# Kernel optimization log

Measured on AMD Instinct MI355X. Metric: run time of the kernel, lower is better.

## Reference

```python
import jax, jax.numpy as jnp
import numpy as np

B, L, D = 8, 2048, 512


def setup_inputs() -> dict:
    key = jax.random.key(0)
    ks = jax.random.split(key, 9)
    s = 1.0 / np.sqrt(D)
    x = jax.random.normal(ks[0], (B, L, D), dtype=jnp.float32)
    Wq = jax.random.uniform(ks[1], (D, D), jnp.float32, -s, s)
    bq = jax.random.uniform(ks[2], (D,), jnp.float32, -s, s)
    Wk = jax.random.uniform(ks[3], (D, D), jnp.float32, -s, s)
    bk = jax.random.uniform(ks[4], (D,), jnp.float32, -s, s)
    Wv = jax.random.uniform(ks[5], (D, D), jnp.float32, -s, s)
    bv = jax.random.uniform(ks[6], (D,), jnp.float32, -s, s)
    Wo = jax.random.uniform(ks[7], (D, D), jnp.float32, -s, s)
    bo = jax.random.uniform(ks[8], (D,), jnp.float32, -s, s)
    return {"x": x, "Wq": Wq, "bq": bq, "Wk": Wk, "bk": bk,
            "Wv": Wv, "bv": bv, "Wo": Wo, "bo": bo}


def reference(x, Wq, bq, Wk, bk, Wv, bv, Wo, bo):
    # Projections then rfft along sequence axis -> complex [B, F, D], F = L//2+1
    Q = jnp.fft.rfft(x @ Wq + bq, axis=1)
    K = jnp.fft.rfft(x @ Wk + bk, axis=1)
    V = jnp.fft.rfft(x @ Wv + bv, axis=1)
    scale = K.shape[-1] ** (-0.5)
    # Complex attention scores over frequency bins: [B, F, F]
    att = jnp.einsum('bfd,bgd->bfg', Q, K) * scale
    attn = jax.nn.softmax(jnp.abs(att), axis=-1)
    context = jnp.einsum('bfg,bgd->bfd', attn.astype(Q.dtype), V)
    context = jnp.fft.irfft(context, n=x.shape[1], axis=1)  # [B, L, D] real
    return context @ Wo + bo
```

## Files before the change

kernel.cpp:

```cpp
#include <hip/hip_runtime.h>
#include <hip/hip_bf16.h>
#include <math.h>

typedef __hip_bfloat16 bf16;
typedef __attribute__((ext_vector_type(8))) short short8;
typedef __attribute__((ext_vector_type(4))) float f32x4;

#define BB 8
#define LL 2048
#define DD 512
#define FF 1025
#define GP 1088
#define FPAD 1152
#define PSTRIDE 589824
#define ATT_SCALE 0.04419417382415922f

__device__ __forceinline__ float b2f(bf16 v) { return __bfloat162float(v); }
__device__ __forceinline__ bf16  f2b(float v) { return __float2bfloat16(v); }
__device__ __forceinline__ float s2f(short s) { bf16 t; *reinterpret_cast<short*>(&t) = s; return b2f(t); }
__device__ __forceinline__ unsigned pk2f(float a, float b) {
    bf16 ha = f2b(a), hb = f2b(b);
    return (unsigned)*(unsigned short*)&ha | ((unsigned)*(unsigned short*)&hb << 16);
}

#define MFMA16(a, b, c) __builtin_amdgcn_mfma_f32_16x16x32_bf16((a), (b), (c), 0, 0, 0)

__device__ __forceinline__ short8 neg8(short8 v) {
    short8 r;
    #pragma unroll
    for (int t = 0; t < 8; ++t) r[t] = (short)(v[t] ^ (short)0x8000);
    return r;
}

typedef __attribute__((address_space(1))) const unsigned int gu32;
typedef __attribute__((address_space(3))) unsigned int lu32;
__device__ __forceinline__ void gl16(const void* g, void* l) {
    __builtin_amdgcn_global_load_lds((gu32*)g, (lu32*)l, 16, 0, 0);
}

template<bool F32>
__device__ __forceinline__ float ldin(const void* p, size_t i) {
    if (F32) return ((const float*)p)[i];
    else     return b2f(((const bf16*)p)[i]);
}

__global__ __launch_bounds__(256) void detect_dtype(const unsigned short* __restrict__ x,
                                                    int* __restrict__ flag)
{
    __shared__ int cnt[256];
    int c = 0;
    for (int i = threadIdx.x; i < 4096; i += 256) {
        const int e = (x[i] >> 7) & 0xFF;
        c += (e >= 100 && e <= 150) ? 1 : 0;
    }
    cnt[threadIdx.x] = c;
    __syncthreads();
    for (int s = 128; s; s >>= 1) {
        if (threadIdx.x < s) cnt[threadIdx.x] += cnt[threadIdx.x + s];
        __syncthreads();
    }
    if (threadIdx.x == 0) *flag = (cnt[0] < 3400) ? 1 : 0;
}

__global__ __launch_bounds__(256) void prep_bias(const void* __restrict__ b0,
                                                 const void* __restrict__ b1,
                                                 const void* __restrict__ b2,
                                                 const void* __restrict__ b3,
                                                 float* __restrict__ bias_f,
                                                 const int* __restrict__ flag)
{
    const int idx = blockIdx.x * 256 + threadIdx.x;
    const int which = idx >> 9, i = idx & 511;
    const void* src = which == 0 ? b0 : (which == 1 ? b1 : (which == 2 ? b2 : b3));
    bias_f[idx] = (*flag) ? ldin<true>(src, i) : ldin<false>(src, i);
}

__global__ __launch_bounds__(256) void split_w_t(const void* __restrict__ W0,
                                                 const void* __restrict__ W1,
                                                 const void* __restrict__ W2,
                                                 const void* __restrict__ W3,
                                                 bf16* __restrict__ WT,
                                                 const int* __restrict__ flag)
{
    const int z = blockIdx.z;
    const void* W = z == 0 ? W0 : (z == 1 ? W1 : (z == 2 ? W2 : W3));
    bf16* Wh = WT + (size_t)z * 524288;
    const int k0 = blockIdx.x * 32, n0 = blockIdx.y * 32;
    const bool f32 = (*flag) != 0;
    __shared__ float Tl[32][33];
    for (int it = 0; it < 4; ++it) {
        const int idx = it * 256 + threadIdx.x;
        const int lk = idx >> 5, ln = idx & 31;
        Tl[lk][ln] = f32 ? ldin<true>(W, (size_t)(k0 + lk) * 512 + n0 + ln)
                         : ldin<false>(W, (size_t)(k0 + lk) * 512 + n0 + ln);
    }
    __syncthreads();
    for (int it = 0; it < 4; ++it) {
        const int idx = it * 256 + threadIdx.x;
        const int ln = idx >> 5, lk = idx & 31;
        Wh[(size_t)(n0 + ln) * 512 + k0 + lk] = f2b(Tl[lk][ln]);
    }
}

__device__ __forceinline__ int shx(int i, int c) {
    const int x = (i << 2) | c;
    return x ^ (((x >> 6) & 3) << 2);
}

__device__ __forceinline__ void fft_decode(int flat, int& b, int& dp) {
    const int c8 = flat & 7;
    const int s  = (flat >> 3) & 1;
    const int pp = flat >> 4;
    const int idx = c8 * 32 + pp;
    b  = idx >> 5;
    dp = ((idx & 31) << 1) | s;
}

__device__ __forceinline__ void fill_twl(float2* twl, int tid) {
    for (int idx = tid; idx < 2047; idx += 512) {
        const int l2 = 31 - __builtin_clz((unsigned)(2047 - idx));
        const int m = 1 << l2;
        const int k = idx - 2048 + 2 * m;
        float s, c2;
        __sincosf(-3.14159265358979f * (float)k / (float)m, &s, &c2);
        twl[idx] = make_float2(c2, s);
    }
}

__global__ __launch_bounds__(512) void rfft_x(const void* __restrict__ x,
                                              bf16* __restrict__ Xh,
                                              const int* __restrict__ flag)
{
    int b, dp;
    fft_decode(blockIdx.x, b, dp);
    const int d0 = dp * 8;
    __shared__ float2 sh[8192];
    __shared__ float2 twl[2048];
    const int tid = threadIdx.x;
    const int c = tid & 3;

    if (*flag) {
        const float* base = (const float*)x + (size_t)b * 2048 * 512 + d0;
        #pragma unroll
        for (int it = 0; it < 8; ++it) {
            const int idx = it * 512 + tid;
            const int l = idx >> 1, fq = idx & 1;
            const float4 v = *(const float4*)(base + (size_t)l * 512 + fq * 4);
            sh[shx(l, fq * 2)]     = make_float2(v.x, v.y);
            sh[shx(l, fq * 2 + 1)] = make_float2(v.z, v.w);
        }
    } else {
        const bf16* base = (const bf16*)x + (size_t)b * 2048 * 512 + d0;
        #pragma unroll
        for (int it = 0; it < 4; ++it) {
            const int l = it * 512 + tid;
            const short8 v = *(const short8*)(base + (size_t)l * 512);
            #pragma unroll
            for (int q = 0; q < 4; ++q)
                sh[shx(l, q)] = make_float2(s2f(v[2 * q]), s2f(v[2 * q + 1]));
        }
    }
    fill_twl(twl, tid);
    __syncthreads();

    const int jb = tid >> 2;
    #pragma unroll
    for (int lsm = 10; lsm >= 0; --lsm) {
        const int m = 1 << lsm;
        const int base = 2048 - (m << 1);
        #pragma unroll
        for (int r = 0; r < 8; ++r) {
            const int j  = jb + 128 * r;
            const int k  = j & (m - 1);
            const int i1 = ((j & ~(m - 1)) << 1) | k;
            const int i2 = i1 + m;
            const float2 w = twl[base + k];
            const float cw = w.x, sw = w.y;
            const float2 a  = sh[shx(i1, c)];
            const float2 bb = sh[shx(i2, c)];
            sh[shx(i1, c)] = make_float2(a.x + bb.x, a.y + bb.y);
            const float dx = a.x - bb.x, dy = a.y - bb.y;
            sh[shx(i2, c)] = make_float2(dx * cw - dy * sw, dx * sw + dy * cw);
        }
        __syncthreads();
    }

    const int fb = tid >> 2;
    const size_t pan_re = (size_t)(b * 64 + dp) * FPAD;
    const size_t pan_im = pan_re + (size_t)512 * FPAD;
    auto dorow = [&](int f) {
        const int rf = __brev((unsigned)f) >> 21;
        const int rc = __brev((unsigned)((2048 - f) & 2047)) >> 21;
        const float2 Zf = sh[shx(rf, c)];
        const float2 Zc = sh[shx(rc, c)];
        const float x1r = 0.5f * (Zf.x + Zc.x);
        const float x1i = 0.5f * (Zf.y - Zc.y);
        const float x2r = 0.5f * (Zf.y + Zc.y);
        const float x2i = -0.5f * (Zf.x - Zc.x);
        const size_t ro_re = (pan_re + f) * 8 + 2 * c;
        const size_t ro_im = (pan_im + f) * 8 + 2 * c;
        *(unsigned*)&Xh[ro_re] = pk2f(x1r, x2r);
        *(unsigned*)&Xh[ro_im] = pk2f(x1i, x2i);
    };
    #pragma unroll
    for (int it = 0; it < 8; ++it)
        dorow(fb * 8 + it);
    if (tid < 4) dorow(1024);

    if (tid < 254) {
        const int f = FF + (tid >> 1);
        const int w = tid & 1;
        const size_t off = (((size_t)(w * 512 + b * 64 + dp)) * FPAD + f) * 8;
        short8 z = {};
        *(short8*)&Xh[off] = z;
    }
}

__global__ __launch_bounds__(256, 4) void proj_all(const bf16* __restrict__ Xh,
                                                   const bf16* __restrict__ WT,
                                                   const float* __restrict__ bias_f,
                                                   bf16* __restrict__ Q,
                                                   bf16* __restrict__ K,
                                                   bf16* __restrict__ Vct)
{
    const int flat = blockIdx.x;
    const bool isV = flat < 576;
    int t, ny, z;
    if (isV) { t = flat >> 2; ny = flat & 3; z = 2; }
    else { const int idx = flat - 576; t = idx >> 3; z = (idx >> 2) & 1; ny = idx & 3; }

    const int pb = t / 9;
    const int f0 = (t - pb * 9) * 128;
    const int plane = pb >> 3, b = pb & 7;
    const int n0 = ny * 128;
    const int tid = threadIdx.x, wv = tid >> 6, lane = tid & 63;
    const int wm = (wv >> 1) * 64, wn = (wv & 1) * 64;
    const size_t pbase = (size_t)pb * PSTRIDE;

    const bf16* Bh = WT + (size_t)z * 524288;
    const float* bias = bias_f + z * 512;

    __shared__ __align__(1024) bf16 SH[16384];
    typedef bf16 (*t64)[64];
    t64 Al = (t64)SH;
    t64 Bl = (t64)(SH + 8192);

    const int r8 = lane >> 3;
    const int sl = lane & 7;
    const int q  = sl ^ r8;
    const int r16 = lane & 15, cc = lane >> 4;
    const int rs8 = r16 & 7;
    const int nn2 = lane & 15, rq = (lane >> 4) * 4;

    f32x4 acc[4][4] = {};
    for (int kt = 0; kt < 512; kt += 64) {
        #pragma unroll
        for (int c2 = 0; c2 < 4; ++c2) {
            const int chunk = wv * 4 + c2;
            const int row = chunk * 8 + r8;
            gl16(&Xh[pbase + ((size_t)((kt >> 3) + q) * FPAD + f0 + row) * 8],
                 (char*)SH + chunk * 1024);
            gl16(&Bh[(size_t)(n0 + row) * 512 + kt + q * 8],
                 (char*)SH + 16384 + chunk * 1024);
        }
        __syncthreads();

        #pragma unroll
        for (int kk = 0; kk < 2; ++kk) {
            short8 af[4], bfr[4];
            const int sa = ((kk * 4 + cc) ^ rs8) * 8;
            #pragma unroll
            for (int i = 0; i < 4; ++i) {
                af[i]  = *(const short8*)&Al[wm + i * 16 + r16][sa];
                bfr[i] = *(const short8*)&Bl[wn + i * 16 + r16][sa];
            }
            #pragma unroll
            for (int i = 0; i < 4; ++i)
                #pragma unroll
                for (int j = 0; j < 4; ++j)
                    acc[i][j] = MFMA16(af[i], bfr[j], acc[i][j]);
        }
        __syncthreads();
    }

    if (!isV) {
        bf16* dst = z == 0 ? Q : K;
        const size_t SPQ = (size_t)BB * FF * DD;
        #pragma unroll
        for (int i = 0; i < 4; ++i)
            #pragma unroll
            for (int j = 0; j < 4; ++j) {
                const int col = n0 + wn + j * 16 + nn2;
                #pragma unroll
                for (int r = 0; r < 4; ++r) {
                    const int f = f0 + wm + i * 16 + rq + r;
                    if (f < FF) {
                        float v = acc[i][j][r];
                        if (plane == 0 && f == 0) v += 2048.0f * bias[col];
                        const int swz = ((f >> 1) & 3) << 3;
                        dst[(size_t)plane * SPQ + ((size_t)(b * FF + f)) * 512 + (col ^ swz)] = f2b(v);
                    }
                }
            }
    } else {
        bf16* T = SH;
        #pragma unroll
        for (int i = 0; i < 4; ++i)
            #pragma unroll
            for (int j = 0; j < 4; ++j) {
                const int col_l = wn + j * 16 + nn2;
                #pragma unroll
                for (int r = 0; r < 4; ++r) {
                    const int row_l = wm + i * 16 + rq + r;
                    const int f = f0 + row_l;
                    float v = (f < FF) ? acc[i][j][r] : 0.f;
                    if (plane == 0 && f == 0) v += 2048.0f * bias[n0 + col_l];
                    T[col_l * 128 + (row_l ^ ((col_l & 15) << 3))] = f2b(v);
                }
            }
        __syncthreads();

        const int nl = tid >> 1, half = tid & 1;
        const size_t gbase = ((size_t)(b * 1024 + plane * 512 + n0 + nl)) * GP + f0;
        #pragma unroll
        for (int a = 0; a < 8; ++a) {
            const int fl = half * 64 + a * 8;
            if (f0 + fl < GP) {
                const short8 v8 = *(const short8*)&T[nl * 128 + (fl ^ ((nl & 15) << 3))];
                *(short8*)&Vct[gbase + fl] = v8;
            }
        }
    }
}

__global__ __launch_bounds__(256, 2) void att_mfma(const bf16* __restrict__ Asp,
                                                   const bf16* __restrict__ Bsp,
                                                   float* __restrict__ att)
{
    const size_t SP = (size_t)BB * FF * DD;
    const int flat = blockIdx.x;
    const int b    = flat & 7;
    const int slot = flat >> 3;
    const int grp  = slot / 51;
    const int rem  = slot % 51;
    const int g    = rem / 3;
    const int r3   = rem % 3;
    const int ft   = grp * 3 + r3;
    const int f0 = ft * 128, g0 = g * 64;

    const int tid = threadIdx.x;
    const int wv = tid >> 6, lane = tid & 63;
    const int wvf = wv >> 1, wvg = wv & 1;

    __shared__ __align__(1024) char LB[49152];

    f32x4 accr[4][2] = {}; f32x4 acci[4][2] = {};

    const int r16 = lane & 15, cc = lane >> 4;
    const int rpos = (cc ^ ((r16 >> 1) & 3)) * 8;
    const size_t abase = (size_t)(b * FF + f0) * 512;
    const size_t bbase = (size_t)(b * FF + g0) * 512;
    const int lrow = lane >> 2;
    const int lcol = (lane & 3) * 8;

    for (int kt = 0; kt < 512; kt += 64) {
        #pragma unroll
        for (int c2 = 0; c2 < 8; ++c2) {
            const int chunk = wv * 8 + c2;
            const int half = chunk >> 4;
            const int pl = (chunk >> 3) & 1, rg = chunk & 7;
            const int row = rg * 16 + lrow;
            gl16(&Asp[(size_t)pl * SP + abase + (size_t)row * 512 + kt + half * 32 + lcol],
                 LB + half * 16384 + ((pl << 3) | rg) * 1024);
        }
        #pragma unroll
        for (int c2 = 0; c2 < 4; ++c2) {
            const int chunk = wv * 4 + c2;
            const int half = chunk >> 3;
            const int pl = (chunk >> 2) & 1, rg = chunk & 3;
            const int row = rg * 16 + lrow;
            gl16(&Bsp[(size_t)pl * SP + bbase + (size_t)row * 512 + kt + half * 32 + lcol],
                 LB + 32768 + half * 8192 + ((pl << 2) | rg) * 1024);
        }
        __syncthreads();

        #pragma unroll
        for (int kk = 0; kk < 2; ++kk) {
            bf16 (*Al)[128][32] = (bf16(*)[128][32])(LB + kk * 16384);
            bf16 (*Bl)[64][32]  = (bf16(*)[64][32])(LB + 32768 + kk * 8192);
            short8 aA[4][2], bB[2][2], nb[2];
            #pragma unroll
            for (int i = 0; i < 4; ++i) {
                const int row = wvf * 64 + i * 16 + r16;
                #pragma unroll
                for (int pl = 0; pl < 2; ++pl)
                    aA[i][pl] = *(const short8*)&Al[pl][row][rpos];
            }
            #pragma unroll
            for (int j = 0; j < 2; ++j) {
                const int row = wvg * 32 + j * 16 + r16;
                #pragma unroll
                for (int pl = 0; pl < 2; ++pl)
                    bB[j][pl] = *(const short8*)&Bl[pl][row][rpos];
                nb[j] = neg8(bB[j][1]);
            }
            #pragma unroll
            for (int i = 0; i < 4; ++i)
                #pragma unroll
                for (int j = 0; j < 2; ++j) {
                    accr[i][j] = MFMA16(aA[i][0], bB[j][0], accr[i][j]);
                    accr[i][j] = MFMA16(aA[i][1], nb[j],    accr[i][j]);
                    acci[i][j] = MFMA16(aA[i][0], bB[j][1], acci[i][j]);
                    acci[i][j] = MFMA16(aA[i][1], bB[j][0], acci[i][j]);
                }
        }
        __syncthreads();
    }

    const int rq = (lane >> 4) * 4;
    #pragma unroll
    for (int i = 0; i < 4; ++i)
        #pragma unroll
        for (int j = 0; j < 2; ++j)
            #pragma unroll
            for (int r = 0; r < 4; ++r) {
                const int f = f0 + wvf * 64 + i * 16 + rq + r;
                const int gg = g0 + wvg * 32 + j * 16 + r16;
                if (f < FF && gg < FF) {
                    const float ar = accr[i][j][r];
                    const float ai = acci[i][j][r];
                    att[((size_t)(b * FF + f)) * FF + gg] = ATT_SCALE * sqrtf(ar * ar + ai * ai);
                }
            }
}

__global__ __launch_bounds__(256) void softmax_rows(const float* __restrict__ att,
                                                    bf16* __restrict__ att16)
{
    const int row = blockIdx.x;
    const float* p = att + (size_t)row * FF;
    bf16* q = att16 + (size_t)row * GP;
    const int tid = threadIdx.x;
    const int lane = tid & 63, wid = tid >> 6;
    __shared__ float srow[1028];
    __shared__ float red[4];

    float m = -1e30f;
    for (int i = tid; i < FF; i += 256) {
        const float v = p[i];
        srow[i] = v;
        m = fmaxf(m, v);
    }
    #pragma unroll
    for (int o = 32; o; o >>= 1) m = fmaxf(m, __shfl_down(m, o));
    if (lane == 0) red[wid] = m;
    __syncthreads();
    m = fmaxf(fmaxf(red[0], red[1]), fmaxf(red[2], red[3]));
    __syncthreads();

    float s = 0.f;
    for (int i = tid; i < FF; i += 256) {
        const float e = expf(srow[i] - m);
        srow[i] = e;
        s += e;
    }
    #pragma unroll
    for (int o = 32; o; o >>= 1) s += __shfl_down(s, o);
    if (lane == 0) red[wid] = s;
    __syncthreads();
    s = red[0] + red[1] + red[2] + red[3];
    const float inv = 1.f / s;
    for (int i = tid; i < GP; i += 256)
        q[i] = f2b(i < FF ? srow[i] * inv : 0.f);
}

__global__ __launch_bounds__(256, 2) void ctx_mfma(const bf16* __restrict__ att16,
                                                   const bf16* __restrict__ Vct,
                                                   bf16* __restrict__ Csp)
{
    const int flat = blockIdx.x;
    const int b    = flat & 7;
    const int slot = flat >> 3;
    const int ft   = slot >> 4;
    const int nt   = slot & 15;
    const int f0 = ft * 128, n0 = nt * 64;

    const int tid = threadIdx.x;
    const int wv = tid >> 6, lane = tid & 63;
    const int wvf = wv >> 1, wvg = wv & 1;

    __shared__ __align__(1024) bf16 SH[12288];
    typedef bf16 (*t64)[64];
    t64 Al = (t64)SH;
    t64 Bl = (t64)(SH + 8192);

    f32x4 acc[4][2] = {};
    const int r8 = lane >> 3, sl = lane & 7, q = sl ^ r8;
    const int r16 = lane & 15, cc = lane >> 4;
    const int rs8 = r16 & 7;

    for (int kt = 0; kt < GP; kt += 64) {
        #pragma unroll
        for (int c2 = 0; c2 < 4; ++c2) {
            const int chunk = wv * 4 + c2;
            const int row = chunk * 8 + r8;
            gl16(&att16[((size_t)(b * FF + f0 + row)) * GP + kt + q * 8],
                 (char*)SH + chunk * 1024);
        }
        #pragma unroll
        for (int c2 = 0; c2 < 2; ++c2) {
            const int chunk = wv * 2 + c2;
            const int row = chunk * 8 + r8;
            gl16(&Vct[((size_t)(b * 1024 + n0 + row)) * GP + kt + q * 8],
                 (char*)SH + 16384 + chunk * 1024);
        }
        __syncthreads();

        #pragma unroll
        for (int kk = 0; kk < 2; ++kk) {
            short8 aA[4], bB[2];
            const int sa = ((kk * 4 + cc) ^ rs8) * 8;
            #pragma unroll
            for (int i = 0; i < 4; ++i)
                aA[i] = *(const short8*)&Al[wvf * 64 + i * 16 + r16][sa];
            #pragma unroll
            for (int j = 0; j < 2; ++j)
                bB[j] = *(const short8*)&Bl[wvg * 32 + j * 16 + r16][sa];
            #pragma unroll
            for (int i = 0; i < 4; ++i)
                #pragma unroll
                for (int j = 0; j < 2; ++j)
                    acc[i][j] = MFMA16(aA[i], bB[j], acc[i][j]);
        }
        __syncthreads();
    }

    const int rq = (lane >> 4) * 4;
    #pragma unroll
    for (int i = 0; i < 4; ++i)
        #pragma unroll
        for (int j = 0; j < 2; ++j)
            #pragma unroll
            for (int r = 0; r < 4; ++r) {
                const int f = f0 + wvf * 64 + i * 16 + rq + r;
                const int n = n0 + wvg * 32 + j * 16 + r16;
                if (f < FF) {
                    const int d = n & 511, pl = n >> 9;
                    Csp[((size_t)(pl * 8 + b) * FPAD + f) * 512 + d] = f2b(acc[i][j][r]);
                }
            }
}

__global__ __launch_bounds__(256) void out_mfma_freq(const bf16* __restrict__ A,
                                                     const bf16* __restrict__ BhT,
                                                     float* __restrict__ CwR,
                                                     float* __restrict__ CwI)
{
    const int t = blockIdx.x;
    const int pb = t / 9;
    const int f0 = (t - pb * 9) * 128;
    const int plane = pb >> 3, b = pb & 7;
    const int m0 = t * 128, n0 = blockIdx.y * 64;
    const int tid = threadIdx.x, wv = tid >> 6, lane = tid & 63;
    const int wvf = wv >> 1, wvg = wv & 1;

    __shared__ __align__(1024) bf16 SH[12288];
    typedef bf16 (*t64)[64];
    t64 Al = (t64)SH;
    t64 Bl = (t64)(SH + 8192);

    f32x4 acc[4][2] = {};
    const int r8 = lane >> 3, sl = lane & 7, q = sl ^ r8;
    const int r16 = lane & 15, cc = lane >> 4;
    const int rs8 = r16 & 7;

    for (int kt = 0; kt < 512; kt += 64) {
        #pragma unroll
        for (int c2 = 0; c2 < 4; ++c2) {
            const int chunk = wv * 4 + c2;
            const int row = chunk * 8 + r8;
            gl16(&A[(size_t)(m0 + row) * 512 + kt + q * 8],
                 (char*)SH + chunk * 1024);
        }
        #pragma unroll
        for (int c2 = 0; c2 < 2; ++c2) {
            const int chunk = wv * 2 + c2;
            const int row = chunk * 8 + r8;
            gl16(&BhT[(size_t)(n0 + row) * 512 + kt + q * 8],
                 (char*)SH + 16384 + chunk * 1024);
        }
        __syncthreads();

        #pragma unroll
        for (int kk = 0; kk < 2; ++kk) {
            short8 af[4], bfr[2];
            const int sa = ((kk * 4 + cc) ^ rs8) * 8;
            #pragma unroll
            for (int i = 0; i < 4; ++i)
                af[i] = *(const short8*)&Al[wvf * 64 + i * 16 + r16][sa];
            #pragma unroll
            for (int j = 0; j < 2; ++j)
                bfr[j] = *(const short8*)&Bl[wvg * 32 + j * 16 + r16][sa];
            #pragma unroll
            for (int i = 0; i < 4; ++i)
                #pragma unroll
                for (int j = 0; j < 2; ++j)
                    acc[i][j] = MFMA16(af[i], bfr[j], acc[i][j]);
        }
        __syncthreads();
    }

    float* dst = plane ? CwI : CwR;
    const int nn2 = lane & 15, rq = (lane >> 4) * 4;
    #pragma unroll
    for (int i = 0; i < 4; ++i)
        #pragma unroll
        for (int j = 0; j < 2; ++j) {
            const int col = n0 + wvg * 32 + j * 16 + nn2;
            #pragma unroll
            for (int r = 0; r < 4; ++r) {
                const int f = f0 + wvf * 64 + i * 16 + rq + r;
                if (f < FF)
                    dst[((size_t)(b * FF + f)) * 512 + col] = acc[i][j][r];
            }
        }
}

__global__ __launch_bounds__(512) void irfft8(const float* __restrict__ CwR,
                                              const float* __restrict__ CwI,
                                              void* __restrict__ out,
                                              const float* __restrict__ bias_f,
                                              const int* __restrict__ flag)
{
    int b, dp;
    fft_decode(blockIdx.x, b, dp);
    const int d0 = dp * 8;
    __shared__ float2 sh[8192];
    __shared__ float2 twl[2048];
    const int tid = threadIdx.x;
    const int c = tid & 3, fb = tid >> 2;

    for (int it = 0; it < 9; ++it) {
        const int f = fb + 128 * it;
        if (f < FF) {
            const size_t off = ((size_t)(b * FF + f)) * 512 + d0 + 2 * c;
            const float2 vr = *(const float2*)(CwR + off);
            const float2 vi = *(const float2*)(CwI + off);
            float c1x = vr.x, c1y = vi.x, c2x = vr.y, c2y = vi.y;
            if (f == 0 || f == 1024) { c1y = 0.f; c2y = 0.f; }
            sh[shx(f, c)] = make_float2(c1x - c2y, c1y + c2x);
            if (f >= 1 && f <= 1023)
                sh[shx(2048 - f, c)] = make_float2(c1x + c2y, c2x - c1y);
        }
    }
    fill_twl(twl, tid);
    __syncthreads();

    const int jb = fb;
    #pragma unroll
    for (int lsm = 10; lsm >= 0; --lsm) {
        const int m = 1 << lsm;
        const int base = 2048 - (m << 1);
        #pragma unroll
        for (int r = 0; r < 8; ++r) {
            const int j  = jb + 128 * r;
            const int k  = j & (m - 1);
            const int i1 = ((j & ~(m - 1)) << 1) | k;
            const int i2 = i1 + m;
            const float2 w = twl[base + k];
            const float cw = w.x, sw = -w.y;
            const float2 a  = sh[shx(i1, c)];
            const float2 bb = sh[shx(i2, c)];
            sh[shx(i1, c)] = make_float2(a.x + bb.x, a.y + bb.y);
            const float dx = a.x - bb.x, dy = a.y - bb.y;
            sh[shx(i2, c)] = make_float2(dx * cw - dy * sw, dx * sw + dy * cw);
        }
        __syncthreads();
    }

    const float sc = 1.0f / 2048.0f;
    const float bo0 = bias_f[1536 + d0 + 2 * c];
    const float bo1 = bias_f[1536 + d0 + 2 * c + 1];
    const bool f32o = (*flag) != 0;
    const int lb = tid >> 2;
    #pragma unroll
    for (int it = 0; it < 16; ++it) {
        const int l  = lb * 16 + it;
        const int rl = __brev((unsigned)l) >> 21;
        const float2 z = sh[shx(rl, c)];
        const float o0 = z.x * sc + bo0;
        const float o1 = z.y * sc + bo1;
        const size_t off = ((size_t)(b * 2048 + l)) * 512 + d0 + 2 * c;
        if (f32o) {
            *(float2*)((float*)out + off) = make_float2(o0, o1);
        } else {
            __hip_bfloat162 h;
            h.x = f2b(o0); h.y = f2b(o1);
            *(__hip_bfloat162*)((bf16*)out + off) = h;
        }
    }
}

extern "C" void kernel_launch(void* const* d_in, const int* in_sizes, int n_in,
                              void* d_out, int out_size, void* d_ws, size_t ws_size,
                              hipStream_t stream)
{
    const void* x  = d_in[0];
    const void* Wq = d_in[1]; const void* bq = d_in[2];
    const void* Wk = d_in[3]; const void* bk = d_in[4];
    const void* Wv = d_in[5]; const void* bv = d_in[6];
    const void* Wo = d_in[7]; const void* bo = d_in[8];

    char* ws = (char*)d_ws;
    char* pA = ws;
    char* pB = pA + 33652736;
    char* pC = pB + 37748736;
    char* pD = pC + 17039360;
    char* pE = pD + 17039360;
    char* pW = pE + 17825792;

    float*  attn = (float*)pA;
    bf16*   Xh   = (bf16*)pB;
    bf16*   att16= (bf16*)pB;
    bf16*   Csp  = (bf16*)(pB + 17843200);
    bf16*   Asp  = (bf16*)pC;
    bf16*   Bsp  = (bf16*)pD;
    float*  CwR  = (float*)pC;
    float*  CwI  = (float*)pD;
    bf16*   Vct  = (bf16*)pE;
    bf16*   WT   = (bf16*)pW;
    float*  bias_f = (float*)(pW + 4194304);
    int*    flag = (int*)(pW + 4194304 + 8192);

    detect_dtype<<<1, 256, 0, stream>>>((const unsigned short*)x, flag);
    prep_bias<<<8, 256, 0, stream>>>(bq, bk, bv, bo, bias_f, flag);
    split_w_t<<<dim3(16, 16, 4), 256, 0, stream>>>(Wq, Wk, Wv, Wo, WT, flag);
    rfft_x<<<dim3(512), 512, 0, stream>>>(x, Xh, flag);
    proj_all<<<dim3(1728), 256, 0, stream>>>(Xh, WT, bias_f, Asp, Bsp, Vct);
    att_mfma<<<dim3(1224), 256, 0, stream>>>(Asp, Bsp, attn);
    softmax_rows<<<dim3(BB * FF), 256, 0, stream>>>(attn, att16);
    ctx_mfma<<<dim3(1152), 256, 0, stream>>>(att16, Vct, Csp);
    out_mfma_freq<<<dim3(144, 8), 256, 0, stream>>>(Csp, WT + 3 * 524288, CwR, CwI);
    irfft8<<<dim3(512), 512, 0, stream>>>(CwR, CwI, d_out, bias_f, flag);
}
```

Baseline: 320.8 us.

## Double-buffer LDS tiles in projection, context and output GEMM kernels

```diff
diff --git a/kernel.cpp b/kernel.cpp
--- a/kernel.cpp
+++ b/kernel.cpp
@@ -216,7 +216,7 @@
     }
 }
 
-__global__ __launch_bounds__(256, 4) void proj_all(const bf16* __restrict__ Xh,
+__global__ __launch_bounds__(256, 2) void proj_all(const bf16* __restrict__ Xh,
                                                    const bf16* __restrict__ WT,
                                                    const float* __restrict__ bias_f,
                                                    bf16* __restrict__ Q,
@@ -240,10 +240,7 @@
     const bf16* Bh = WT + (size_t)z * 524288;
     const float* bias = bias_f + z * 512;
 
-    __shared__ __align__(1024) bf16 SH[16384];
-    typedef bf16 (*t64)[64];
-    t64 Al = (t64)SH;
-    t64 Bl = (t64)(SH + 8192);
+    __shared__ __align__(1024) bf16 SH[32768];
 
     const int r8 = lane >> 3;
     const int sl = lane & 7;
@@ -252,27 +249,41 @@
     const int rs8 = r16 & 7;
     const int nn2 = lane & 15, rq = (lane >> 4) * 4;
 
-    f32x4 acc[4][4] = {};
-    for (int kt = 0; kt < 512; kt += 64) {
+    auto STAGE = [&](int buf, int kt) {
+        char* base = (char*)SH + buf * 32768;
         #pragma unroll
         for (int c2 = 0; c2 < 4; ++c2) {
             const int chunk = wv * 4 + c2;
             const int row = chunk * 8 + r8;
             gl16(&Xh[pbase + ((size_t)((kt >> 3) + q) * FPAD + f0 + row) * 8],
-                 (char*)SH + chunk * 1024);
+                 base + chunk * 1024);
             gl16(&Bh[(size_t)(n0 + row) * 512 + kt + q * 8],
-                 (char*)SH + 16384 + chunk * 1024);
-        }
-        __syncthreads();
-
+                 base + 16384 + chunk * 1024);
+        }
+    };
+
+    f32x4 acc[4][4] = {};
+    STAGE(0, 0);
+    for (int it = 0; it < 8; ++it) {
+        if (it < 7) {
+            STAGE((it + 1) & 1, (it + 1) * 64);
+            asm volatile("s_waitcnt vmcnt(8)" ::: "memory");
+        } else {
+            asm volatile("s_waitcnt vmcnt(0)" ::: "memory");
+        }
+        __builtin_amdgcn_s_barrier();
+        __builtin_amdgcn_sched_barrier(0);
+
+        const bf16* Ab = SH + (it & 1) * 16384;
+        const bf16* Bb = Ab + 8192;
         #pragma unroll
         for (int kk = 0; kk < 2; ++kk) {
             short8 af[4], bfr[4];
             const int sa = ((kk * 4 + cc) ^ rs8) * 8;
             #pragma unroll
             for (int i = 0; i < 4; ++i) {
-                af[i]  = *(const short8*)&Al[wm + i * 16 + r16][sa];
-                bfr[i] = *(const short8*)&Bl[wn + i * 16 + r16][sa];
+                af[i]  = *(const short8*)&Ab[(wm + i * 16 + r16) * 64 + sa];
+                bfr[i] = *(const short8*)&Bb[(wn + i * 16 + r16) * 64 + sa];
             }
             #pragma unroll
             for (int i = 0; i < 4; ++i)
@@ -280,7 +291,8 @@
                 for (int j = 0; j < 4; ++j)
                     acc[i][j] = MFMA16(af[i], bfr[j], acc[i][j]);
         }
-        __syncthreads();
+        asm volatile("s_waitcnt lgkmcnt(0)" ::: "memory");
+        __builtin_amdgcn_s_barrier();
     }
 
     if (!isV) {
@@ -489,50 +501,62 @@
     const int wv = tid >> 6, lane = tid & 63;
     const int wvf = wv >> 1, wvg = wv & 1;
 
-    __shared__ __align__(1024) bf16 SH[12288];
-    typedef bf16 (*t64)[64];
-    t64 Al = (t64)SH;
-    t64 Bl = (t64)(SH + 8192);
+    __shared__ __align__(1024) bf16 SH[24576];
 
     f32x4 acc[4][2] = {};
     const int r8 = lane >> 3, sl = lane & 7, q = sl ^ r8;
     const int r16 = lane & 15, cc = lane >> 4;
     const int rs8 = r16 & 7;
 
-    for (int kt = 0; kt < GP; kt += 64) {
+    auto STAGE = [&](int buf, int kt) {
+        char* base = (char*)SH + buf * 24576;
         #pragma unroll
         for (int c2 = 0; c2 < 4; ++c2) {
             const int chunk = wv * 4 + c2;
             const int row = chunk * 8 + r8;
             gl16(&att16[((size_t)(b * FF + f0 + row)) * GP + kt + q * 8],
-                 (char*)SH + chunk * 1024);
+                 base + chunk * 1024);
         }
         #pragma unroll
         for (int c2 = 0; c2 < 2; ++c2) {
             const int chunk = wv * 2 + c2;
             const int row = chunk * 8 + r8;
             gl16(&Vct[((size_t)(b * 1024 + n0 + row)) * GP + kt + q * 8],
-                 (char*)SH + 16384 + chunk * 1024);
-        }
-        __syncthreads();
-
+                 base + 16384 + chunk * 1024);
+        }
+    };
+
+    STAGE(0, 0);
+    for (int it = 0; it < 17; ++it) {
+        if (it < 16) {
+            STAGE((it + 1) & 1, (it + 1) * 64);
+            asm volatile("s_waitcnt vmcnt(6)" ::: "memory");
+        } else {
+            asm volatile("s_waitcnt vmcnt(0)" ::: "memory");
+        }
+        __builtin_amdgcn_s_barrier();
+        __builtin_amdgcn_sched_barrier(0);
+
+        const bf16* Ab = SH + (it & 1) * 12288;
+        const bf16* Bb = Ab + 8192;
         #pragma unroll
         for (int kk = 0; kk < 2; ++kk) {
             short8 aA[4], bB[2];
             const int sa = ((kk * 4 + cc) ^ rs8) * 8;
             #pragma unroll
             for (int i = 0; i < 4; ++i)
-                aA[i] = *(const short8*)&Al[wvf * 64 + i * 16 + r16][sa];
+                aA[i] = *(const short8*)&Ab[(wvf * 64 + i * 16 + r16) * 64 + sa];
             #pragma unroll
             for (int j = 0; j < 2; ++j)
-                bB[j] = *(const short8*)&Bl[wvg * 32 + j * 16 + r16][sa];
+                bB[j] = *(const short8*)&Bb[(wvg * 32 + j * 16 + r16) * 64 + sa];
             #pragma unroll
             for (int i = 0; i < 4; ++i)
                 #pragma unroll
                 for (int j = 0; j < 2; ++j)
                     acc[i][j] = MFMA16(aA[i], bB[j], acc[i][j]);
         }
-        __syncthreads();
+        asm volatile("s_waitcnt lgkmcnt(0)" ::: "memory");
+        __builtin_amdgcn_s_barrier();
     }
 
     const int rq = (lane >> 4) * 4;
@@ -551,10 +575,10 @@
             }
 }
 
-__global__ __launch_bounds__(256) void out_mfma_freq(const bf16* __restrict__ A,
-                                                     const bf16* __restrict__ BhT,
-                                                     float* __restrict__ CwR,
-                                                     float* __restrict__ CwI)
+__global__ __launch_bounds__(256, 2) void out_mfma_freq(const bf16* __restrict__ A,
+                                                        const bf16* __restrict__ BhT,
+                                                        float* __restrict__ CwR,
+                                                        float* __restrict__ CwI)
 {
     const int t = blockIdx.x;
     const int pb = t / 9;
@@ -564,50 +588,62 @@
     const int tid = threadIdx.x, wv = tid >> 6, lane = tid & 63;
     const int wvf = wv >> 1, wvg = wv & 1;
 
-    __shared__ __align__(1024) bf16 SH[12288];
-    typedef bf16 (*t64)[64];
-    t64 Al = (t64)SH;
-    t64 Bl = (t64)(SH + 8192);
+    __shared__ __align__(1024) bf16 SH[24576];
 
     f32x4 acc[4][2] = {};
     const int r8 = lane >> 3, sl = lane & 7, q = sl ^ r8;
     const int r16 = lane & 15, cc = lane >> 4;
     const int rs8 = r16 & 7;
 
-    for (int kt = 0; kt < 512; kt += 64) {
+    auto STAGE = [&](int buf, int kt) {
+        char* base = (char*)SH + buf * 24576;
         #pragma unroll
         for (int c2 = 0; c2 < 4; ++c2) {
             const int chunk = wv * 4 + c2;
             const int row = chunk * 8 + r8;
             gl16(&A[(size_t)(m0 + row) * 512 + kt + q * 8],
-                 (char*)SH + chunk * 1024);
+                 base + chunk * 1024);
         }
         #pragma unroll
         for (int c2 = 0; c2 < 2; ++c2) {
             const int chunk = wv * 2 + c2;
             const int row = chunk * 8 + r8;
             gl16(&BhT[(size_t)(n0 + row) * 512 + kt + q * 8],
-                 (char*)SH + 16384 + chunk * 1024);
-        }
-        __syncthreads();
-
+                 base + 16384 + chunk * 1024);
+        }
+    };
+
+    STAGE(0, 0);
+    for (int it = 0; it < 8; ++it) {
+        if (it < 7) {
+            STAGE((it + 1) & 1, (it + 1) * 64);
+            asm volatile("s_waitcnt vmcnt(6)" ::: "memory");
+        } else {
+            asm volatile("s_waitcnt vmcnt(0)" ::: "memory");
+        }
+        __builtin_amdgcn_s_barrier();
+        __builtin_amdgcn_sched_barrier(0);
+
+        const bf16* Ab = SH + (it & 1) * 12288;
+        const bf16* Bb = Ab + 8192;
         #pragma unroll
         for (int kk = 0; kk < 2; ++kk) {
             short8 af[4], bfr[2];
             const int sa = ((kk * 4 + cc) ^ rs8) * 8;
             #pragma unroll
             for (int i = 0; i < 4; ++i)
-                af[i] = *(const short8*)&Al[wvf * 64 + i * 16 + r16][sa];
+                af[i] = *(const short8*)&Ab[(wvf * 64 + i * 16 + r16) * 64 + sa];
             #pragma unroll
             for (int j = 0; j < 2; ++j)
-                bfr[j] = *(const short8*)&Bl[wvg * 32 + j * 16 + r16][sa];
+                bfr[j] = *(const short8*)&Bb[(wvg * 32 + j * 16 + r16) * 64 + sa];
             #pragma unroll
             for (int i = 0; i < 4; ++i)
                 #pragma unroll
                 for (int j = 0; j < 2; ++j)
                     acc[i][j] = MFMA16(af[i], bfr[j], acc[i][j]);
         }
-        __syncthreads();
+        asm volatile("s_waitcnt lgkmcnt(0)" ::: "memory");
+        __builtin_amdgcn_s_barrier();
     }
 
     float* dst = plane ? CwI : CwR;
```

Result: faster. 305.8 us (-4.6%).
